# Performance work log

Hardware: AMD Instinct MI355X
Metric: run time of the kernel (lower is better)

## Reference

```python
import jax, jax.numpy as jnp
import numpy as np

B, C, IH, IW = 16, 512, 28, 28
HEADS, DIM_HEAD = 8, 32
INNER = HEADS * DIM_HEAD            # 256
HIDDEN = 4 * C                      # 2048
N = IH * IW                         # 784 tokens
EPS = 1e-5


def _relative_index(ih, iw):
    coords = np.stack(np.meshgrid(np.arange(ih), np.arange(iw), indexing='ij')).reshape(2, -1)
    rel = coords[:, :, None] - coords[:, None, :]
    rel[0] += ih - 1
    rel[1] += iw - 1
    rel[0] *= 2 * iw - 1
    return jnp.asarray((rel[0] + rel[1]).reshape(-1))  # (n*n,)

REL_IDX = _relative_index(IH, IW)


def _layernorm(x, g, b):
    mu = jnp.mean(x, axis=-1, keepdims=True)
    var = jnp.mean(jnp.square(x - mu), axis=-1, keepdims=True)
    return (x - mu) * jax.lax.rsqrt(var + EPS) * g + b


def setup_inputs() -> dict:
    key = jax.random.key(0)
    ks = jax.random.split(key, 12)
    s = lambda fan_in: 1.0 / np.sqrt(fan_in)
    return {
        'x': jax.random.normal(ks[0], (B, C, IH, IW), jnp.float32),
        'ln1_g': jnp.ones((C,), jnp.float32),
        'ln1_b': jnp.zeros((C,), jnp.float32),
        'qkv_w': jax.random.normal(ks[1], (C, 3 * INNER), jnp.float32) * s(C),
        'qkv_b': jnp.zeros((3 * INNER,), jnp.float32),
        'out_w': jax.random.normal(ks[2], (INNER, C), jnp.float32) * s(INNER),
        'out_b': jnp.zeros((C,), jnp.float32),
        'rel_table': jax.random.normal(ks[3], ((2 * IH - 1) * (2 * IW - 1), HEADS), jnp.float32) * 0.02,
        'ln2_g': jnp.ones((C,), jnp.float32),
        'ln2_b': jnp.zeros((C,), jnp.float32),
        'ff_w1': jax.random.normal(ks[4], (C, HIDDEN), jnp.float32) * s(C),
        'ff_b1': jnp.zeros((HIDDEN,), jnp.float32),
        'ff_w2': jax.random.normal(ks[5], (HIDDEN, C), jnp.float32) * s(HIDDEN),
        'ff_b2': jnp.zeros((C,), jnp.float32),
    }


def reference(x, ln1_g, ln1_b, qkv_w, qkv_b, out_w, out_b, rel_table,
              ln2_g, ln2_b, ff_w1, ff_b1, ff_w2, ff_b2):
    scale = DIM_HEAD ** -0.5
    # b c h w -> b n c
    xs = x.reshape(B, C, N).transpose(0, 2, 1)

    # --- PreNorm attention branch ---
    h = _layernorm(xs, ln1_g, ln1_b)
    qkv = h @ qkv_w + qkv_b                               # [B, N, 3*INNER]
    q, k, v = jnp.split(qkv, 3, axis=-1)
    split_heads = lambda t: t.reshape(B, N, HEADS, DIM_HEAD).transpose(0, 2, 1, 3)
    q, k, v = map(split_heads, (q, k, v))                 # [B, H, N, d]
    dots = jnp.einsum('bhnd,bhmd->bhnm', q, k) * scale    # [B, H, N, N]
    bias = rel_table[REL_IDX].reshape(N, N, HEADS).transpose(2, 0, 1)  # [H, N, N]
    attn = jax.nn.softmax(dots + bias[None], axis=-1)
    o = jnp.einsum('bhnm,bhmd->bhnd', attn, v)            # [B, H, N, d]
    o = o.transpose(0, 2, 1, 3).reshape(B, N, INNER)
    o = o @ out_w + out_b                                 # [B, N, C]
    xs = xs + o                                           # residual

    # --- PreNorm FFN branch ---
    h = _layernorm(xs, ln2_g, ln2_b)
    h = jax.nn.gelu(h @ ff_w1 + ff_b1, approximate=False)
    h = h @ ff_w2 + ff_b2
    xs = xs + h

    # b n c -> b c h w
    return xs.transpose(0, 2, 1).reshape(B, C, IH, IW)
```

## Files before the change

### kernel.cpp

```cpp
#include <hip/hip_runtime.h>
#include <hip/hip_bf16.h>

#define DEVI __device__ __forceinline__

typedef __attribute__((ext_vector_type(8))) short bf16x8;
typedef __attribute__((ext_vector_type(4))) float f32x4;
typedef __attribute__((ext_vector_type(2))) unsigned u32x2;

static constexpr int BB = 16, CC = 512, NT = 784, HD = 8, DH = 32;
static constexpr int INNER = 256, HID = 2048, MTOT = BB * NT;

DEVI short f2bf(float x) {
  unsigned u = __builtin_bit_cast(unsigned, x);
  u += 0x7fffu + ((u >> 16) & 1u);
  return (short)(u >> 16);
}

DEVI void gll16(const void* g, void* l) {
  __builtin_amdgcn_global_load_lds(
      (const __attribute__((address_space(1))) unsigned int*)g,
      (__attribute__((address_space(3))) unsigned int*)l, 16, 0, 0);
}

__device__ void wprep_body(const float* __restrict__ W, short* __restrict__ WT,
                           int K0, int N0, int bx, int by, float* smem) {
  float (*tile)[33] = (float(*)[33])smem;
  const int tk0 = bx * 32, tn0 = by * 32;
  const int tx = threadIdx.x & 31, ty = threadIdx.x >> 5;
#pragma unroll
  for (int i = 0; i < 4; ++i)
    tile[ty + i * 8][tx] = W[(size_t)(tk0 + ty + i * 8) * N0 + tn0 + tx];
  __syncthreads();
#pragma unroll
  for (int i = 0; i < 4; ++i)
    WT[(size_t)(tn0 + ty + i * 8) * K0 + tk0 + tx] = f2bf(tile[tx][ty + i * 8]);
}

__global__ void prep_kernel(const float* __restrict__ qkv_w, short* __restrict__ wqkvT,
                            const float* __restrict__ out_w, short* __restrict__ woutT,
                            const float* __restrict__ ff_w1, short* __restrict__ wf1T,
                            const float* __restrict__ ff_w2, short* __restrict__ wf2T,
                            const float* __restrict__ x, float* __restrict__ xs,
                            const float* __restrict__ rel, short* __restrict__ bt) {
  __shared__ float smem[64 * 17];
  const int bid = blockIdx.x;
  if (bid < 384) {
    wprep_body(qkv_w, wqkvT, 512, 768, bid & 15, bid >> 4, smem);
  } else if (bid < 512) {
    int l = bid - 384;
    wprep_body(out_w, woutT, 256, 512, l & 7, l >> 3, smem);
  } else if (bid < 1536) {
    int l = bid - 512;
    wprep_body(ff_w1, wf1T, 512, 2048, l & 15, l >> 4, smem);
  } else if (bid < 2560) {
    int l = bid - 1536;
    wprep_body(ff_w2, wf2T, 2048, 512, l & 63, l >> 6, smem);
  } else if (bid < 8832) {
    int l = bid - 2560;
    float (*tile)[17] = (float(*)[17])smem;
    const int n0 = (l % 49) * 16, c0 = ((l / 49) & 7) * 64, b = l / 392;
    const int tx = threadIdx.x & 15, ty = threadIdx.x >> 4;
    const float* p = x + ((size_t)b * CC + c0) * NT + n0;
#pragma unroll
    for (int i = 0; i < 4; ++i)
      tile[ty + i * 16][tx] = p[(size_t)(ty + i * 16) * NT + tx];
    __syncthreads();
    float* qd = xs + ((size_t)b * NT + n0) * CC + c0;
    const int cx = threadIdx.x & 63, ny = threadIdx.x >> 6;
#pragma unroll
    for (int i = 0; i < 4; ++i)
      qd[(size_t)(ny + i * 4) * CC + cx] = tile[cx][ny + i * 4];
  } else {
    int id = (bid - 8832) * 256 + threadIdx.x;
    int r = id & 3;
    int lane = (id >> 2) & 63;
    int wid = (id >> 8) & 3;
    int t = id >> 10;
    int jhi = t % 49;
    int t2 = t / 49;
    int qc = t2 % 13;
    int h = t2 / 13;
    int i = qc * 64 + wid * 16 + ((lane >> 4) << 2) + r;
    if (i > 783) i = 783;
    int j = jhi * 16 + (lane & 15);
    int hi_ = i / 28, wi_ = i - hi_ * 28;
    int hj = j / 28, wj = j - hj * 28;
    int ridx = (hi_ - hj + 27) * 55 + (wi_ - wj + 27);
    bt[id] = f2bf(rel[ridx * 8 + h] * 1.4426950408889634f);
  }
}

__global__ void ln_kernel(const float* __restrict__ in, const float* __restrict__ gw,
                          const float* __restrict__ bw, short* __restrict__ h_out) {
  int t = blockIdx.x;
  int tid = threadIdx.x;
  const float* p = in + (size_t)t * CC;
  float v0 = p[tid], v1 = p[tid + 256];
  float s = v0 + v1, s2 = v0 * v0 + v1 * v1;
#pragma unroll
  for (int m = 1; m < 64; m <<= 1) {
    s += __shfl_xor(s, m);
    s2 += __shfl_xor(s2, m);
  }
  __shared__ float red[8];
  int wid = tid >> 6;
  if ((tid & 63) == 0) { red[wid] = s; red[4 + wid] = s2; }
  __syncthreads();
  s = red[0] + red[1] + red[2] + red[3];
  s2 = red[4] + red[5] + red[6] + red[7];
  float mu = s * (1.f / 512.f);
  float var = s2 * (1.f / 512.f) - mu * mu;
  float rs = rsqrtf(var + 1e-5f);
  h_out[(size_t)t * CC + tid] = f2bf((v0 - mu) * rs * gw[tid] + bw[tid]);
  h_out[(size_t)t * CC + tid + 256] = f2bf((v1 - mu) * rs * gw[tid + 256] + bw[tid + 256]);
}

template <int EPI, int BM, int BN, int MINW>
__global__ __launch_bounds__(256, MINW) void gemm_bt(
    const short* __restrict__ A, const short* __restrict__ BT,
    const float* __restrict__ bias, int K, void* __restrict__ out0,
    void* __restrict__ o1, void* __restrict__ o2, const float* __restrict__ res,
    int Nld, int nn) {
  __shared__ short As[BM * 64];
  __shared__ short Bs[BN * 64];
  const int tid = threadIdx.x;
  const int lane = tid & 63, wid = tid >> 6;
  const int nwg = gridDim.x, orig = blockIdx.x;
  const int q = nwg >> 3, rm = nwg & 7;
  const int xcd = orig & 7, idx = orig >> 3;
  const int wg = (xcd < rm) ? (xcd * (q + 1) + idx)
                            : (rm * (q + 1) + (xcd - rm) * q + idx);
  const int mt = wg / nn, nt = wg - mt * nn;
  const int m0 = mt * BM, n0 = nt * BN;
  const int wm = wid >> 1, wn = wid & 1;
  constexpr int MF = BM >> 5;
  constexpr int NF = BN >> 5;
  constexpr int ACALLS = BM / 32;
  constexpr int BCALLS = BN / 32;
  const int lg = lane >> 4, ln = lane & 15;

  f32x4 acc[MF][NF] = {};
  for (int kt = 0; kt < K; kt += 64) {
#pragma unroll
    for (int call = 0; call < ACALLS; ++call) {
      int cb = call * 256 + (wid << 6);
      int c = cb + lane;
      int row = c >> 3, j8 = c & 7;
      gll16(A + (size_t)(m0 + row) * K + kt + (j8 ^ (row & 7)) * 8, &As[cb * 8]);
    }
#pragma unroll
    for (int call = 0; call < BCALLS; ++call) {
      int cb = call * 256 + (wid << 6);
      int c = cb + lane;
      int row = c >> 3, j8 = c & 7;
      gll16(BT + (size_t)(n0 + row) * K + kt + (j8 ^ (row & 7)) * 8, &Bs[cb * 8]);
    }
    __syncthreads();
#pragma unroll
    for (int kk = 0; kk < 64; kk += 32) {
      bf16x8 af[MF], bfr[NF];
#pragma unroll
      for (int mf = 0; mf < MF; ++mf) {
        int r = wm * (BM >> 1) + mf * 16 + ln;
        af[mf] = *(const bf16x8*)&As[r * 64 + ((((kk >> 3) + lg) ^ (r & 7)) << 3)];
      }
#pragma unroll
      for (int nf = 0; nf < NF; ++nf) {
        int r = wn * (BN >> 1) + nf * 16 + ln;
        bfr[nf] = *(const bf16x8*)&Bs[r * 64 + ((((kk >> 3) + lg) ^ (r & 7)) << 3)];
      }
#pragma unroll
      for (int mf = 0; mf < MF; ++mf)
#pragma unroll
        for (int nf = 0; nf < NF; ++nf)
          acc[mf][nf] = __builtin_amdgcn_mfma_f32_16x16x32_bf16(af[mf], bfr[nf], acc[mf][nf], 0, 0, 0);
    }
    __syncthreads();
  }
#pragma unroll
  for (int mf = 0; mf < MF; ++mf)
#pragma unroll
    for (int nf = 0; nf < NF; ++nf) {
      int col = n0 + wn * (BN >> 1) + nf * 16 + ln;
      float bv = bias[col];
#pragma unroll
      for (int r = 0; r < 4; ++r) {
        int row = m0 + wm * (BM >> 1) + mf * 16 + lg * 4 + r;
        float val = acc[mf][nf][r] + bv;
        if (EPI == 0) {
          int which = col >> 8, head = (col >> 5) & 7, dd = col & 31;
          int b = row / NT, n = row - b * NT;
          if (which == 2) {
            ((short*)o2)[((size_t)((b * HD + head) * DH + dd)) * NT + n] = f2bf(val);
          } else {
            short* dst = (which == 0) ? (short*)out0 : (short*)o1;
            dst[((size_t)((b * HD + head) * NT + n)) * DH + dd] = f2bf(val);
          }
        } else if (EPI == 1) {
          ((float*)out0)[(size_t)row * Nld + col] = val + res[(size_t)row * Nld + col];
        } else if (EPI == 2) {
          float v2 = val * val;
          float y = val * fmaf(0.102944458f, v2, 2.30225813f);
          y = fminf(y, 80.f);
          float e = __builtin_amdgcn_exp2f(y);
          float gl = val * e * __builtin_amdgcn_rcpf(e + 1.0f);
          ((short*)out0)[(size_t)row * Nld + col] = f2bf(gl);
        } else {
          int b = row / NT, n = row - b * NT;
          ((float*)out0)[((size_t)(b * CC + col)) * NT + n] =
              val + res[(size_t)row * Nld + col];
        }
      }
    }
}

__global__ __launch_bounds__(256, 3) void attn_kernel(
    const short* __restrict__ qb, const short* __restrict__ kb,
    const short* __restrict__ vtg, const short* __restrict__ bt,
    short* __restrict__ ob) {
  const int qc = blockIdx.x;
  const int bh = blockIdx.y;
  const int b = bh >> 3, h = bh & 7;
  const int tid = threadIdx.x, lane = tid & 63, wid = tid >> 6;
  const int lg = lane >> 4, ln = lane & 15;
  const int rb = qc * 64 + wid * 16;
  const float SC2 = 0.17677669529663687f * 1.4426950408889634f;

  __shared__ short Pl[4][16 * 136];
  short* pw = Pl[wid];

  const short* qrow = qb + (size_t)bh * NT * DH;
  bf16x8 aq;
  {
    int r = rb + ln;
    if (r > 783) r = 783;
    aq = *(const bf16x8*)(qrow + (size_t)r * DH + lg * 8);
  }
  float l_run[4] = {};
  f32x4 o_acc[2] = {};
  const short* kbase = kb + (size_t)bh * NT * DH;
  const short* vbase = vtg + (size_t)bh * DH * NT;
  const short* btw = bt + ((size_t)(h * 13 + qc) * 49) * 1024 + wid * 256 + lane * 4;

  bf16x8 kcur[8];
#pragma unroll
  for (int nf = 0; nf < 8; ++nf)
    kcur[nf] = *(const bf16x8*)(kbase + (size_t)(nf * 16 + ln) * DH + lg * 8);

  for (int jt = 0; jt < 768; jt += 128) {
    const int jt0 = jt >> 4;
    bf16x8 knext[8];
#pragma unroll
    for (int nf = 0; nf < 8; ++nf) {
      int j = jt + 128 + nf * 16 + ln;
      if (j > 783) j = 783;
      knext[nf] = *(const bf16x8*)(kbase + (size_t)j * DH + lg * 8);
    }
    bf16x8 vreg[4][2];
#pragma unroll
    for (int kk = 0; kk < 4; ++kk)
#pragma unroll
      for (int dr = 0; dr < 2; ++dr)
        vreg[kk][dr] = *(const bf16x8*)(vbase + (size_t)(dr * 16 + ln) * NT + jt + kk * 32 + lg * 8);

#pragma unroll
    for (int nf = 0; nf < 8; ++nf) {
      const u32x2 bq = *(const u32x2*)(btw + (size_t)(jt0 + nf) * 1024);
      f32x4 zr = {0.f, 0.f, 0.f, 0.f};
      f32x4 s = __builtin_amdgcn_mfma_f32_16x16x32_bf16(aq, kcur[nf], zr, 0, 0, 0);
      unsigned w0 = bq.x, w1 = bq.y;
      float p0 = __builtin_amdgcn_exp2f(fmaf(s[0], SC2, __builtin_bit_cast(float, w0 << 16)));
      float p1 = __builtin_amdgcn_exp2f(fmaf(s[1], SC2, __builtin_bit_cast(float, w0 & 0xffff0000u)));
      float p2 = __builtin_amdgcn_exp2f(fmaf(s[2], SC2, __builtin_bit_cast(float, w1 << 16)));
      float p3 = __builtin_amdgcn_exp2f(fmaf(s[3], SC2, __builtin_bit_cast(float, w1 & 0xffff0000u)));
      l_run[0] += p0;
      l_run[1] += p1;
      l_run[2] += p2;
      l_run[3] += p3;
      int pa = (lg * 4) * 136 + nf * 16 + ln;
      pw[pa] = f2bf(p0);
      pw[pa + 136] = f2bf(p1);
      pw[pa + 272] = f2bf(p2);
      pw[pa + 408] = f2bf(p3);
    }
#pragma unroll
    for (int kk = 0; kk < 4; ++kk) {
      bf16x8 ap = *(const bf16x8*)&pw[ln * 136 + kk * 32 + lg * 8];
#pragma unroll
      for (int dr = 0; dr < 2; ++dr)
        o_acc[dr] = __builtin_amdgcn_mfma_f32_16x16x32_bf16(ap, vreg[kk][dr], o_acc[dr], 0, 0, 0);
    }
#pragma unroll
    for (int nf = 0; nf < 8; ++nf) kcur[nf] = knext[nf];
  }

  {
    {
      int pa = (lg * 4) * 136 + 16 + ln;
#pragma unroll
      for (int r = 0; r < 4; ++r) pw[pa + r * 136] = 0;
    }
    const u32x2 bq = *(const u32x2*)(btw + (size_t)48 * 1024);
    f32x4 zr = {0.f, 0.f, 0.f, 0.f};
    f32x4 s = __builtin_amdgcn_mfma_f32_16x16x32_bf16(aq, kcur[0], zr, 0, 0, 0);
    unsigned w0 = bq.x, w1 = bq.y;
    float p0 = __builtin_amdgcn_exp2f(fmaf(s[0], SC2, __builtin_bit_cast(float, w0 << 16)));
    float p1 = __builtin_amdgcn_exp2f(fmaf(s[1], SC2, __builtin_bit_cast(float, w0 & 0xffff0000u)));
    float p2 = __builtin_amdgcn_exp2f(fmaf(s[2], SC2, __builtin_bit_cast(float, w1 << 16)));
    float p3 = __builtin_amdgcn_exp2f(fmaf(s[3], SC2, __builtin_bit_cast(float, w1 & 0xffff0000u)));
    l_run[0] += p0;
    l_run[1] += p1;
    l_run[2] += p2;
    l_run[3] += p3;
    int pa = (lg * 4) * 136 + ln;
    pw[pa] = f2bf(p0);
    pw[pa + 136] = f2bf(p1);
    pw[pa + 272] = f2bf(p2);
    pw[pa + 408] = f2bf(p3);
    {
      bf16x8 ap = *(const bf16x8*)&pw[ln * 136 + lg * 8];
      bf16x8 bv[2];
#pragma unroll
      for (int dr = 0; dr < 2; ++dr) {
        int col = 768 + lg * 8;
        if (col < NT)
          bv[dr] = *(const bf16x8*)(vbase + (size_t)(dr * 16 + ln) * NT + col);
        else {
          bf16x8 zz = {};
          bv[dr] = zz;
        }
      }
#pragma unroll
      for (int dr = 0; dr < 2; ++dr)
        o_acc[dr] = __builtin_amdgcn_mfma_f32_16x16x32_bf16(ap, bv[dr], o_acc[dr], 0, 0, 0);
    }
  }

#pragma unroll
  for (int msk = 1; msk < 16; msk <<= 1)
#pragma unroll
    for (int r = 0; r < 4; ++r) l_run[r] += __shfl_xor(l_run[r], msk);

  float rinv[4];
#pragma unroll
  for (int r = 0; r < 4; ++r) rinv[r] = 1.0f / l_run[r];
#pragma unroll
  for (int dr = 0; dr < 2; ++dr)
#pragma unroll
    for (int r = 0; r < 4; ++r) {
      int row = rb + lg * 4 + r;
      if (row < 784) {
        float val = o_acc[dr][r] * rinv[r];
        ob[((size_t)(b * NT + row)) * INNER + h * DH + dr * 16 + ln] = f2bf(val);
      }
    }
}

extern "C" void kernel_launch(void* const* d_in, const int* in_sizes, int n_in,
                              void* d_out, int out_size, void* d_ws, size_t ws_size,
                              hipStream_t stream) {
  const float* x = (const float*)d_in[0];
  const float* ln1_g = (const float*)d_in[1];
  const float* ln1_b = (const float*)d_in[2];
  const float* qkv_w = (const float*)d_in[3];
  const float* qkv_b = (const float*)d_in[4];
  const float* out_w = (const float*)d_in[5];
  const float* out_b = (const float*)d_in[6];
  const float* rel_table = (const float*)d_in[7];
  const float* ln2_g = (const float*)d_in[8];
  const float* ln2_b = (const float*)d_in[9];
  const float* ff_w1 = (const float*)d_in[10];
  const float* ff_b1 = (const float*)d_in[11];
  const float* ff_w2 = (const float*)d_in[12];
  const float* ff_b2 = (const float*)d_in[13];
  float* out = (float*)d_out;
  char* ws = (char*)d_ws;

  constexpr size_t OFF_XS = 0;
  constexpr size_t OFF_H = 25690112;
  constexpr size_t OFF_WQKV = 38535168;
  constexpr size_t OFF_WOUT = 39321600;
  constexpr size_t OFF_WF1 = 39583744;
  constexpr size_t OFF_WF2 = 41680896;
  constexpr size_t OFF_Q = 43778048;
  constexpr size_t OFF_K = 50200576;
  constexpr size_t OFF_VT = 63045632;
  constexpr size_t OFF_O = 69468160;
  constexpr size_t OFF_XS2 = 75890688;
  constexpr size_t OFF_G = 101580800;

  float* xs = (float*)(ws + OFF_XS);
  short* h = (short*)(ws + OFF_H);
  short* wqkvT = (short*)(ws + OFF_WQKV);
  short* woutT = (short*)(ws + OFF_WOUT);
  short* wf1T = (short*)(ws + OFF_WF1);
  short* wf2T = (short*)(ws + OFF_WF2);
  short* qb = (short*)(ws + OFF_Q);
  short* kb = (short*)(ws + OFF_K);
  short* vt = (short*)(ws + OFF_VT);
  short* ob = (short*)(ws + OFF_O);
  short* bt = (short*)(ws + OFF_XS2);
  float* xs2 = (float*)(ws + OFF_XS2);
  short* g = (short*)(ws + OFF_G);

  prep_kernel<<<29216, 256, 0, stream>>>(qkv_w, wqkvT, out_w, woutT,
                                         ff_w1, wf1T, ff_w2, wf2T,
                                         x, xs, rel_table, bt);

  ln_kernel<<<MTOT, 256, 0, stream>>>(xs, ln1_g, ln1_b, h);

  gemm_bt<0, 128, 64, 3><<<1176, 256, 0, stream>>>(h, wqkvT, qkv_b, 512, qb, kb, vt, nullptr, 0, 12);

  attn_kernel<<<dim3(13, 128), 256, 0, stream>>>(qb, kb, vt, bt, ob);

  gemm_bt<1, 128, 64, 3><<<784, 256, 0, stream>>>(ob, woutT, out_b, 256, xs2, nullptr, nullptr, xs, 512, 8);

  ln_kernel<<<MTOT, 256, 0, stream>>>(xs2, ln2_g, ln2_b, h);

  gemm_bt<2, 128, 128, 3><<<1568, 256, 0, stream>>>(h, wf1T, ff_b1, 512, g, nullptr, nullptr, nullptr, 2048, 16);

  gemm_bt<3, 128, 64, 3><<<784, 256, 0, stream>>>(g, wf2T, ff_b2, 2048, out, nullptr, nullptr, xs2, 512, 8);
}
```

Baseline: 223.3 us.

## Double-buffer GEMM LDS tiles with prefetch and shrink FF1 tile to 128x64

The GEMM main loop now uses two LDS buffers. It issues the global-to-LDS loads for tile t+1 before computing tile t, and waits with an explicit vmcnt so memory latency overlaps MFMA work. The FF1 GEMM switches from 128x128 to 128x64 tiles, because the hardcoded vmcnt literal assumes six loads per tile. This doubles its grid and increases B-operand reuse cost. The doubled LDS footprint may lower occupancy, and the hand-written waitcnt ties correctness to the load count.

```diff
diff --git a/kernel.cpp b/kernel.cpp
--- a/kernel.cpp
+++ b/kernel.cpp
@@ -121,8 +121,8 @@
     const float* __restrict__ bias, int K, void* __restrict__ out0,
     void* __restrict__ o1, void* __restrict__ o2, const float* __restrict__ res,
     int Nld, int nn) {
-  __shared__ short As[BM * 64];
-  __shared__ short Bs[BN * 64];
+  __shared__ short As[2][BM * 64];
+  __shared__ short Bs[2][BN * 64];
   const int tid = threadIdx.x;
   const int lane = tid & 63, wid = tid >> 6;
   const int nwg = gridDim.x, orig = blockIdx.x;
@@ -137,37 +137,53 @@
   constexpr int NF = BN >> 5;
   constexpr int ACALLS = BM / 32;
   constexpr int BCALLS = BN / 32;
+  constexpr int NLD = ACALLS + BCALLS;
+  static_assert(NLD == 6, "vmcnt literal assumes 6 loads/tile");
   const int lg = lane >> 4, ln = lane & 15;
 
-  f32x4 acc[MF][NF] = {};
-  for (int kt = 0; kt < K; kt += 64) {
+  auto stage = [&](int buf, int kt) {
 #pragma unroll
     for (int call = 0; call < ACALLS; ++call) {
       int cb = call * 256 + (wid << 6);
       int c = cb + lane;
       int row = c >> 3, j8 = c & 7;
-      gll16(A + (size_t)(m0 + row) * K + kt + (j8 ^ (row & 7)) * 8, &As[cb * 8]);
+      gll16(A + (size_t)(m0 + row) * K + kt + (j8 ^ (row & 7)) * 8, &As[buf][cb * 8]);
     }
 #pragma unroll
     for (int call = 0; call < BCALLS; ++call) {
       int cb = call * 256 + (wid << 6);
       int c = cb + lane;
       int row = c >> 3, j8 = c & 7;
-      gll16(BT + (size_t)(n0 + row) * K + kt + (j8 ^ (row & 7)) * 8, &Bs[cb * 8]);
-    }
-    __syncthreads();
+      gll16(BT + (size_t)(n0 + row) * K + kt + (j8 ^ (row & 7)) * 8, &Bs[buf][cb * 8]);
+    }
+  };
+
+  f32x4 acc[MF][NF] = {};
+  const int nk = K >> 6;
+  stage(0, 0);
+  for (int t = 0; t < nk; ++t) {
+    const int cur = t & 1;
+    if (t + 1 < nk) {
+      stage(cur ^ 1, (t + 1) << 6);
+      asm volatile("s_waitcnt vmcnt(6)" ::: "memory");
+    } else {
+      asm volatile("s_waitcnt vmcnt(0)" ::: "memory");
+    }
+    __builtin_amdgcn_s_barrier();
+    const short* as = As[cur];
+    const short* bs = Bs[cur];
 #pragma unroll
     for (int kk = 0; kk < 64; kk += 32) {
       bf16x8 af[MF], bfr[NF];
 #pragma unroll
       for (int mf = 0; mf < MF; ++mf) {
         int r = wm * (BM >> 1) + mf * 16 + ln;
-        af[mf] = *(const bf16x8*)&As[r * 64 + ((((kk >> 3) + lg) ^ (r & 7)) << 3)];
+        af[mf] = *(const bf16x8*)&as[r * 64 + ((((kk >> 3) + lg) ^ (r & 7)) << 3)];
       }
 #pragma unroll
       for (int nf = 0; nf < NF; ++nf) {
         int r = wn * (BN >> 1) + nf * 16 + ln;
-        bfr[nf] = *(const bf16x8*)&Bs[r * 64 + ((((kk >> 3) + lg) ^ (r & 7)) << 3)];
+        bfr[nf] = *(const bf16x8*)&bs[r * 64 + ((((kk >> 3) + lg) ^ (r & 7)) << 3)];
       }
 #pragma unroll
       for (int mf = 0; mf < MF; ++mf)
@@ -175,7 +191,8 @@
         for (int nf = 0; nf < NF; ++nf)
           acc[mf][nf] = __builtin_amdgcn_mfma_f32_16x16x32_bf16(af[mf], bfr[nf], acc[mf][nf], 0, 0, 0);
     }
-    __syncthreads();
+    __builtin_amdgcn_sched_barrier(0);
+    __builtin_amdgcn_s_barrier();
   }
 #pragma unroll
   for (int mf = 0; mf < MF; ++mf)
@@ -417,7 +434,7 @@
 
   ln_kernel<<<MTOT, 256, 0, stream>>>(xs2, ln2_g, ln2_b, h);
 
-  gemm_bt<2, 128, 128, 3><<<1568, 256, 0, stream>>>(h, wf1T, ff_b1, 512, g, nullptr, nullptr, nullptr, 2048, 16);
+  gemm_bt<2, 128, 64, 3><<<3136, 256, 0, stream>>>(h, wf1T, ff_b1, 512, g, nullptr, nullptr, nullptr, 2048, 32);
 
   gemm_bt<3, 128, 64, 3><<<784, 256, 0, stream>>>(g, wf2T, ff_b2, 2048, out, nullptr, nullptr, xs2, 512, 8);
 }
```

New measurement: 254.8 us. 1.14x slower.

## Transpose QK^T MFMA output so each lane holds one query row

Applied to the files above, without the earlier changes.

Swaps the MFMA operands so S^T is computed, which leaves each lane holding four consecutive key columns for a single query row. The probabilities can then be packed into bf16 pairs and written to LDS as one 8-byte store instead of four scalar 2-byte stores. The row-sum is kept as a single scalar per lane, which replaces the 16-way shuffle reduction with two shuffles plus a broadcast. The precomputed bias layout is permuted to match. This is meant to cut LDS store instructions and reduction work in the attention inner loop, at the cost of a different bias indexing and extra shuffles for the reciprocal.

```diff
diff --git a/kernel.cpp b/kernel.cpp
--- a/kernel.cpp
+++ b/kernel.cpp
@@ -14,6 +14,10 @@
   unsigned u = __builtin_bit_cast(unsigned, x);
   u += 0x7fffu + ((u >> 16) & 1u);
   return (short)(u >> 16);
+}
+
+DEVI unsigned pack2bf(float lo, float hi) {
+  return ((unsigned)(unsigned short)f2bf(lo)) | ((unsigned)(unsigned short)f2bf(hi) << 16);
 }
 
 DEVI void gll16(const void* g, void* l) {
@@ -76,13 +80,13 @@
     int lane = (id >> 2) & 63;
     int wid = (id >> 8) & 3;
     int t = id >> 10;
-    int jhi = t % 49;
+    int jblk = t % 49;
     int t2 = t / 49;
     int qc = t2 % 13;
     int h = t2 / 13;
-    int i = qc * 64 + wid * 16 + ((lane >> 4) << 2) + r;
+    int i = qc * 64 + wid * 16 + (lane & 15);
     if (i > 783) i = 783;
-    int j = jhi * 16 + (lane & 15);
+    int j = jblk * 16 + ((lane >> 4) << 2) + r;
     int hi_ = i / 28, wi_ = i - hi_ * 28;
     int hj = j / 28, wj = j - hj * 28;
     int ridx = (hi_ - hj + 27) * 55 + (wi_ - wj + 27);
@@ -236,7 +240,7 @@
     if (r > 783) r = 783;
     aq = *(const bf16x8*)(qrow + (size_t)r * DH + lg * 8);
   }
-  float l_run[4] = {};
+  float l_acc = 0.f;
   f32x4 o_acc[2] = {};
   const short* kbase = kb + (size_t)bh * NT * DH;
   const short* vbase = vtg + (size_t)bh * DH * NT;
@@ -267,21 +271,15 @@
     for (int nf = 0; nf < 8; ++nf) {
       const u32x2 bq = *(const u32x2*)(btw + (size_t)(jt0 + nf) * 1024);
       f32x4 zr = {0.f, 0.f, 0.f, 0.f};
-      f32x4 s = __builtin_amdgcn_mfma_f32_16x16x32_bf16(aq, kcur[nf], zr, 0, 0, 0);
+      f32x4 s = __builtin_amdgcn_mfma_f32_16x16x32_bf16(kcur[nf], aq, zr, 0, 0, 0);
       unsigned w0 = bq.x, w1 = bq.y;
       float p0 = __builtin_amdgcn_exp2f(fmaf(s[0], SC2, __builtin_bit_cast(float, w0 << 16)));
       float p1 = __builtin_amdgcn_exp2f(fmaf(s[1], SC2, __builtin_bit_cast(float, w0 & 0xffff0000u)));
       float p2 = __builtin_amdgcn_exp2f(fmaf(s[2], SC2, __builtin_bit_cast(float, w1 << 16)));
       float p3 = __builtin_amdgcn_exp2f(fmaf(s[3], SC2, __builtin_bit_cast(float, w1 & 0xffff0000u)));
-      l_run[0] += p0;
-      l_run[1] += p1;
-      l_run[2] += p2;
-      l_run[3] += p3;
-      int pa = (lg * 4) * 136 + nf * 16 + ln;
-      pw[pa] = f2bf(p0);
-      pw[pa + 136] = f2bf(p1);
-      pw[pa + 272] = f2bf(p2);
-      pw[pa + 408] = f2bf(p3);
+      l_acc += (p0 + p1) + (p2 + p3);
+      u32x2 pk = {pack2bf(p0, p1), pack2bf(p2, p3)};
+      *(u32x2*)&pw[ln * 136 + nf * 16 + (lg << 2)] = pk;
     }
 #pragma unroll
     for (int kk = 0; kk < 4; ++kk) {
@@ -296,27 +294,20 @@
 
   {
     {
-      int pa = (lg * 4) * 136 + 16 + ln;
-#pragma unroll
-      for (int r = 0; r < 4; ++r) pw[pa + r * 136] = 0;
+      u32x2 zz = {0u, 0u};
+      *(u32x2*)&pw[ln * 136 + 16 + (lg << 2)] = zz;
     }
     const u32x2 bq = *(const u32x2*)(btw + (size_t)48 * 1024);
     f32x4 zr = {0.f, 0.f, 0.f, 0.f};
-    f32x4 s = __builtin_amdgcn_mfma_f32_16x16x32_bf16(aq, kcur[0], zr, 0, 0, 0);
+    f32x4 s = __builtin_amdgcn_mfma_f32_16x16x32_bf16(kcur[0], aq, zr, 0, 0, 0);
     unsigned w0 = bq.x, w1 = bq.y;
     float p0 = __builtin_amdgcn_exp2f(fmaf(s[0], SC2, __builtin_bit_cast(float, w0 << 16)));
     float p1 = __builtin_amdgcn_exp2f(fmaf(s[1], SC2, __builtin_bit_cast(float, w0 & 0xffff0000u)));
     float p2 = __builtin_amdgcn_exp2f(fmaf(s[2], SC2, __builtin_bit_cast(float, w1 << 16)));
     float p3 = __builtin_amdgcn_exp2f(fmaf(s[3], SC2, __builtin_bit_cast(float, w1 & 0xffff0000u)));
-    l_run[0] += p0;
-    l_run[1] += p1;
-    l_run[2] += p2;
-    l_run[3] += p3;
-    int pa = (lg * 4) * 136 + ln;
-    pw[pa] = f2bf(p0);
-    pw[pa + 136] = f2bf(p1);
-    pw[pa + 272] = f2bf(p2);
-    pw[pa + 408] = f2bf(p3);
+    l_acc += (p0 + p1) + (p2 + p3);
+    u32x2 pk = {pack2bf(p0, p1), pack2bf(p2, p3)};
+    *(u32x2*)&pw[ln * 136 + (lg << 2)] = pk;
     {
       bf16x8 ap = *(const bf16x8*)&pw[ln * 136 + lg * 8];
       bf16x8 bv[2];
@@ -336,14 +327,12 @@
     }
   }
 
-#pragma unroll
-  for (int msk = 1; msk < 16; msk <<= 1)
-#pragma unroll
-    for (int r = 0; r < 4; ++r) l_run[r] += __shfl_xor(l_run[r], msk);
+  l_acc += __shfl_xor(l_acc, 16);
+  l_acc += __shfl_xor(l_acc, 32);
 
   float rinv[4];
 #pragma unroll
-  for (int r = 0; r < 4; ++r) rinv[r] = 1.0f / l_run[r];
+  for (int r = 0; r < 4; ++r) rinv[r] = 1.0f / __shfl(l_acc, lg * 4 + r);
 #pragma unroll
   for (int dr = 0; dr < 2; ++dr)
 #pragma unroll
```

Measured after the change: 223.2 us. No clear change (-0.0%).
